# Kernel optimization log

Hardware: AMD Instinct MI355X
Metric: run time of the kernel (lower is better)

Reference implementation:

```python
import jax, jax.numpy as jnp
import numpy as np

D_K = 128  # query/key dim, used for the 1/sqrt(d_k) scale


def setup_inputs() -> dict:
    key = jax.random.key(0)
    k1, k2, k3, k4 = jax.random.split(key, 4)
    B, L, d_model, d_k, d_v = 4, 2048, 1024, 128, 128

    def xavier(k, shape):
        # matches nn.init.xavier_uniform_ for 2D weights
        limit = np.sqrt(6.0 / (shape[0] + shape[1]))
        return jax.random.uniform(k, shape, jnp.float32, -limit, limit)

    return {
        "X": jax.random.normal(k1, (B, L, d_model), jnp.float32),
        "W_Q": xavier(k2, (d_model, d_k)),
        "W_K": xavier(k3, (d_model, d_k)),
        "W_V": xavier(k4, (d_model, d_v)),
    }


def reference(X, W_Q, W_K, W_V):
    # X: (B, L, d_model)
    L = X.shape[1]
    Q = jnp.einsum("bld,dk->blk", X, W_Q)          # (B, L, d_k)
    K = jnp.einsum("bld,dk->blk", X, W_K)          # (B, L, d_k)
    V = jnp.einsum("bld,dv->blv", X, W_V)          # (B, L, d_v)
    scale = D_K ** -0.5
    scores = jnp.einsum("bqk,bpk->bqp", Q, K) * scale  # (B, L, L)
    # causal mask: positions above the diagonal set to -inf
    causal = jnp.tril(jnp.ones((L, L), dtype=bool))
    scores = jnp.where(causal, scores, -jnp.inf)
    A = jax.nn.softmax(scores, axis=-1)            # (B, L, L)
    Z = jnp.einsum("bqp,bpv->bqv", A, V)           # (B, L, d_v)
    return Z
```

## Files before the change

kernel.cpp:

```cpp
#include <hip/hip_runtime.h>
#include <hip/hip_bf16.h>

typedef __bf16 bf16;
typedef __attribute__((ext_vector_type(4))) __bf16 bf16x4;
typedef __attribute__((ext_vector_type(8))) __bf16 bf16x8;
typedef __attribute__((ext_vector_type(4))) float f32x4;

#define D_MODEL 1024
#define DK 128
#define LSEQ 2048
#define NQT 128
#define NB 4
#define SCALE2 (0.08838834764831845f * 1.4426950408889634f)

__global__ __launch_bounds__(256) void wt_kernel(
    const float* __restrict__ Wq, const float* __restrict__ Wk,
    const float* __restrict__ Wv, bf16* __restrict__ Wt)
{
    __shared__ bf16 tile[64][72];
    const float* W = (blockIdx.z == 0) ? Wq : (blockIdx.z == 1) ? Wk : Wv;
    int k0 = blockIdx.x * 64;
    int n0 = blockIdx.y * 64;
    int t  = threadIdx.x;
    #pragma unroll
    for (int i = 0; i < 16; ++i) {
        int idx = t + i * 256;
        int r = idx >> 6, c = idx & 63;
        tile[c][r] = (bf16)W[(size_t)(k0 + r) * DK + n0 + c];
    }
    __syncthreads();
    bf16* out = Wt + (size_t)blockIdx.z * DK * D_MODEL;
    #pragma unroll
    for (int i = 0; i < 16; ++i) {
        int idx = t + i * 256;
        int rr = idx >> 6, cc = idx & 63;
        out[(size_t)(n0 + rr) * D_MODEL + k0 + cc] = tile[rr][cc];
    }
}

__global__ __launch_bounds__(256) void proj_kernel(
    const float* __restrict__ X, const bf16* __restrict__ Wt,
    bf16* __restrict__ Qs, bf16* __restrict__ Kb, bf16* __restrict__ Vt)
{
    __shared__ bf16 Xs[64][72];
    __shared__ bf16 Ws[128][72];
    int mt = blockIdx.x, mat = blockIdx.y;
    const bf16* W = Wt + (size_t)mat * DK * D_MODEL;
    int t = threadIdx.x;
    int wave = t >> 6, lane = t & 63;
    int lq = lane & 15, g = lane >> 4;
    int row0 = mt * 64;

    f32x4 acc[4][2];
    #pragma unroll
    for (int m = 0; m < 4; ++m)
        #pragma unroll
        for (int n = 0; n < 2; ++n) acc[m][n] = f32x4{0.f, 0.f, 0.f, 0.f};

    f32x4  rxf[4];
    bf16x8 rw[4];
    auto LOADR = [&](int k0) {
        #pragma unroll
        for (int i = 0; i < 4; ++i) {
            int u = t + i * 256, r = u >> 4, c4 = u & 15;
            rxf[i] = *reinterpret_cast<const f32x4*>(
                &X[(size_t)(row0 + r) * D_MODEL + k0 + c4 * 4]);
        }
        #pragma unroll
        for (int i = 0; i < 4; ++i) {
            int u = t + i * 256, r = u >> 3, c8 = u & 7;
            rw[i] = *reinterpret_cast<const bf16x8*>(
                &W[(size_t)r * D_MODEL + k0 + c8 * 8]);
        }
    };
    auto STORER = [&]() {
        #pragma unroll
        for (int i = 0; i < 4; ++i) {
            int u = t + i * 256, r = u >> 4, c4 = u & 15;
            bf16x4 h;
            h[0]=(bf16)rxf[i][0]; h[1]=(bf16)rxf[i][1];
            h[2]=(bf16)rxf[i][2]; h[3]=(bf16)rxf[i][3];
            *reinterpret_cast<bf16x4*>(&Xs[r][c4 * 4]) = h;
        }
        #pragma unroll
        for (int i = 0; i < 4; ++i) {
            int u = t + i * 256, r = u >> 3, c8 = u & 7;
            *reinterpret_cast<bf16x8*>(&Ws[r][c8 * 8]) = rw[i];
        }
    };

    LOADR(0);
    for (int ks = 0; ks < 16; ++ks) {
        __syncthreads();
        STORER();
        if (ks + 1 < 16) LOADR((ks + 1) * 64);
        __syncthreads();
        #pragma unroll
        for (int kk = 0; kk < 2; ++kk) {
            bf16x8 a[4];
            #pragma unroll
            for (int mr = 0; mr < 4; ++mr)
                a[mr] = *reinterpret_cast<const bf16x8*>(&Xs[mr * 16 + lq][kk * 32 + g * 8]);
            #pragma unroll
            for (int n = 0; n < 2; ++n) {
                bf16x8 bfr = *reinterpret_cast<const bf16x8*>(
                    &Ws[wave * 32 + n * 16 + lq][kk * 32 + g * 8]);
                #pragma unroll
                for (int mr = 0; mr < 4; ++mr)
                    acc[mr][n] = __builtin_amdgcn_mfma_f32_16x16x32_bf16(a[mr], bfr, acc[mr][n], 0, 0, 0);
            }
        }
    }
    #pragma unroll
    for (int mr = 0; mr < 4; ++mr) {
        int orow = row0 + mr * 16 + g * 4;
        #pragma unroll
        for (int n = 0; n < 2; ++n) {
            int col = wave * 32 + n * 16 + lq;
            if (mat == 0) {
                #pragma unroll
                for (int r = 0; r < 4; ++r)
                    Qs[(size_t)(orow + r) * DK + col] = (bf16)(acc[mr][n][r] * SCALE2);
            } else if (mat == 1) {
                #pragma unroll
                for (int r = 0; r < 4; ++r)
                    Kb[(size_t)(orow + r) * DK + col] = (bf16)acc[mr][n][r];
            } else {
                int bb  = orow >> 11;
                int kv0 = orow & 2047;
                bf16x4 h;
                h[0]=(bf16)acc[mr][n][0]; h[1]=(bf16)acc[mr][n][1];
                h[2]=(bf16)acc[mr][n][2]; h[3]=(bf16)acc[mr][n][3];
                *reinterpret_cast<bf16x4*>(
                    &Vt[((size_t)bb * DK + col) * LSEQ + kv0]) = h;
            }
        }
    }
}

__global__ __launch_bounds__(256, 3) void attn_kernel(
    const bf16* __restrict__ Qs, const bf16* __restrict__ Kb,
    const bf16* __restrict__ Vt, float* __restrict__ Zp,
    float* __restrict__ Mp, float* __restrict__ Lp,
    float* __restrict__ Out, int S, int direct)
{
    __shared__ bf16 Ks[64][136];
    __shared__ bf16 Vs[128][72];
    __shared__ bf16 P[4][16][72];
    int bid = blockIdx.x;
    int b, qblk, s;
    if (S == 4) {
        int xcd = bid & 7, n = bid >> 3;
        b = xcd >> 1;
        int half = n >> 5, qraw = n & 31;
        qblk = half ? (31 - qraw) : qraw;
        s = ((xcd & 1) << 1) | half;
    } else {
        b = bid / (S * 32);
        int rem = bid % (S * 32);
        qblk = rem & 31;
        s = rem >> 5;
    }
    int t = threadIdx.x;
    int wave = t >> 6, lane = t & 63;
    int lq = lane & 15, g = lane >> 4;
    int qw16 = qblk * 4 + wave;
    int qg = qw16 * 16 + lq;

    int nt  = qblk + 1;
    int cpt = (nt + S - 1) / S;
    int t0  = s * cpt;
    int t1  = min(t0 + cpt, nt);

    const bf16* Kbase = Kb + (size_t)b * LSEQ * DK;
    const bf16* Vbase = Vt + (size_t)b * DK * LSEQ;

    const bf16* Qrow = Qs + ((size_t)b * LSEQ + qg) * DK;
    bf16x8 qf[4];
    #pragma unroll
    for (int ks = 0; ks < 4; ++ks)
        qf[ks] = *reinterpret_cast<const bf16x8*>(&Qrow[ks * 32 + g * 8]);

    f32x4 z[8];
    #pragma unroll
    for (int i = 0; i < 8; ++i) z[i] = f32x4{0.f, 0.f, 0.f, 0.f};
    float mrun = -3.0e38f, lrun = 0.f;

    bf16x8 kreg[4], vreg[4];
    auto LOADKV = [&](int kvb) {
        #pragma unroll
        for (int i = 0; i < 4; ++i) {
            int u = t + i * 256, r = u >> 4, c = u & 15;
            kreg[i] = *reinterpret_cast<const bf16x8*>(
                &Kbase[(size_t)(kvb + r) * DK + c * 8]);
        }
        #pragma unroll
        for (int i = 0; i < 4; ++i) {
            int u = t + i * 256, d = u >> 3, c = u & 7;
            vreg[i] = *reinterpret_cast<const bf16x8*>(
                &Vbase[(size_t)d * LSEQ + kvb + c * 8]);
        }
    };
    auto STOREKV = [&]() {
        #pragma unroll
        for (int i = 0; i < 4; ++i) {
            int u = t + i * 256, r = u >> 4, c = u & 15;
            *reinterpret_cast<bf16x8*>(&Ks[r][c * 8]) = kreg[i];
        }
        #pragma unroll
        for (int i = 0; i < 4; ++i) {
            int u = t + i * 256, d = u >> 3, c = u & 7;
            *reinterpret_cast<bf16x8*>(&Vs[d][c * 8]) = vreg[i];
        }
    };

    if (t0 < t1) {
        LOADKV(t0 * 64);
        for (int ti = t0; ti < t1; ++ti) {
            int kvb = ti * 64;
            __syncthreads();
            STOREKV();
            if (ti + 1 < t1) LOADKV((ti + 1) * 64);
            __syncthreads();

            f32x4 sc[4];
            #pragma unroll
            for (int jj = 0; jj < 4; ++jj) sc[jj] = f32x4{0.f, 0.f, 0.f, 0.f};
            __builtin_amdgcn_s_setprio(1);
            #pragma unroll
            for (int jj = 0; jj < 4; ++jj)
                #pragma unroll
                for (int ks = 0; ks < 4; ++ks) {
                    bf16x8 a = *reinterpret_cast<const bf16x8*>(
                        &Ks[jj * 16 + lq][ks * 32 + g * 8]);
                    sc[jj] = __builtin_amdgcn_mfma_f32_16x16x32_bf16(a, qf[ks], sc[jj], 0, 0, 0);
                }
            __builtin_amdgcn_s_setprio(0);

            float sv[16];
            if (ti == nt - 1) {
                #pragma unroll
                for (int jj = 0; jj < 4; ++jj)
                    #pragma unroll
                    for (int r = 0; r < 4; ++r) {
                        int kv0 = kvb + jj * 16 + g * 4 + r;
                        sv[jj * 4 + r] = (kv0 <= qg) ? sc[jj][r] : -3.0e38f;
                    }
            } else {
                #pragma unroll
                for (int jj = 0; jj < 4; ++jj)
                    #pragma unroll
                    for (int r = 0; r < 4; ++r) sv[jj * 4 + r] = sc[jj][r];
            }
            float mt = sv[0];
            #pragma unroll
            for (int i = 1; i < 16; ++i) mt = fmaxf(mt, sv[i]);
            mt = fmaxf(mt, __shfl_xor(mt, 16));
            mt = fmaxf(mt, __shfl_xor(mt, 32));
            if (!__all(mt <= mrun)) {
                float mnew  = fmaxf(mrun, mt);
                float alpha = exp2f(mrun - mnew);
                lrun *= alpha;
                #pragma unroll
                for (int i = 0; i < 8; ++i) {
                    z[i][0] *= alpha; z[i][1] *= alpha; z[i][2] *= alpha; z[i][3] *= alpha;
                }
                mrun = mnew;
            }
            float psum = 0.f;
            #pragma unroll
            for (int jj = 0; jj < 4; ++jj) {
                bf16x4 pb;
                #pragma unroll
                for (int r = 0; r < 4; ++r) {
                    float e = exp2f(sv[jj * 4 + r] - mrun);
                    psum += e;
                    pb[r] = (bf16)e;
                }
                *reinterpret_cast<bf16x4*>(&P[wave][lq][jj * 16 + g * 4]) = pb;
            }
            psum += __shfl_xor(psum, 16);
            psum += __shfl_xor(psum, 32);
            lrun += psum;
            __builtin_amdgcn_s_setprio(1);
            #pragma unroll
            for (int sl = 0; sl < 2; ++sl) {
                bf16x8 pf = *reinterpret_cast<const bf16x8*>(&P[wave][lq][sl * 32 + g * 8]);
                #pragma unroll
                for (int dt = 0; dt < 8; ++dt) {
                    bf16x8 av = *reinterpret_cast<const bf16x8*>(
                        &Vs[dt * 16 + lq][sl * 32 + g * 8]);
                    z[dt] = __builtin_amdgcn_mfma_f32_16x16x32_bf16(av, pf, z[dt], 0, 0, 0);
                }
            }
            __builtin_amdgcn_s_setprio(0);
        }
    }

    if (direct) {
        float inv = 1.f / lrun;
        float* orow = Out + ((size_t)b * LSEQ + qg) * DK;
        #pragma unroll
        for (int dt = 0; dt < 8; ++dt) {
            f32x4 v;
            v[0]=z[dt][0]*inv; v[1]=z[dt][1]*inv; v[2]=z[dt][2]*inv; v[3]=z[dt][3]*inv;
            *reinterpret_cast<f32x4*>(&orow[dt * 16 + g * 4]) = v;
        }
    } else {
        size_t T = ((size_t)(b * NQT + qw16) * S + s);
        float* zp = Zp + T * (16 * 128);
        #pragma unroll
        for (int dt = 0; dt < 8; ++dt)
            *reinterpret_cast<f32x4*>(&zp[lq * 128 + dt * 16 + g * 4]) = z[dt];
        if (g == 0) {
            Mp[T * 16 + lq] = mrun;
            Lp[T * 16 + lq] = lrun;
        }
    }
}

__global__ __launch_bounds__(256) void combine_kernel(
    const float* __restrict__ Zp, const float* __restrict__ Mp,
    const float* __restrict__ Lp, float* __restrict__ Out, int S)
{
    int qt = blockIdx.x, b = blockIdx.y;
    int t  = threadIdx.x;
    int r  = t >> 4;
    int d0 = (t & 15) * 8;
    size_t Tbase = (size_t)(b * NQT + qt) * S;

    float m = -3.0e38f;
    for (int s = 0; s < S; ++s)
        m = fmaxf(m, Mp[(Tbase + s) * 16 + r]);

    float L = 0.f;
    f32x4 a0 = {0.f,0.f,0.f,0.f}, a1 = {0.f,0.f,0.f,0.f};
    for (int s = 0; s < S; ++s) {
        float w = exp2f(Mp[(Tbase + s) * 16 + r] - m);
        L += w * Lp[(Tbase + s) * 16 + r];
        const float* zp = Zp + (Tbase + s) * (16 * 128) + r * 128 + d0;
        f32x4 v0 = *reinterpret_cast<const f32x4*>(&zp[0]);
        f32x4 v1 = *reinterpret_cast<const f32x4*>(&zp[4]);
        a0[0]+=w*v0[0]; a0[1]+=w*v0[1]; a0[2]+=w*v0[2]; a0[3]+=w*v0[3];
        a1[0]+=w*v1[0]; a1[1]+=w*v1[1]; a1[2]+=w*v1[2]; a1[3]+=w*v1[3];
    }
    float inv = 1.f / L;
    float* orow = Out + ((size_t)b * LSEQ + qt * 16 + r) * DK + d0;
    f32x4 o0, o1;
    o0[0]=a0[0]*inv; o0[1]=a0[1]*inv; o0[2]=a0[2]*inv; o0[3]=a0[3]*inv;
    o1[0]=a1[0]*inv; o1[1]=a1[1]*inv; o1[2]=a1[2]*inv; o1[3]=a1[3]*inv;
    *reinterpret_cast<f32x4*>(&orow[0]) = o0;
    *reinterpret_cast<f32x4*>(&orow[4]) = o1;
}

extern "C" void kernel_launch(void* const* d_in, const int* in_sizes, int n_in,
                              void* d_out, int out_size, void* d_ws, size_t ws_size,
                              hipStream_t stream)
{
    const float* X  = (const float*)d_in[0];
    const float* Wq = (const float*)d_in[1];
    const float* Wk = (const float*)d_in[2];
    const float* Wv = (const float*)d_in[3];
    float* Out = (float*)d_out;

    char* ws = (char*)d_ws;
    bf16* Wt = (bf16*)(ws);
    bf16* Qs = (bf16*)(ws + ((size_t)1 << 20));
    bf16* Kb = (bf16*)(ws + ((size_t)3 << 20));
    bf16* Vt = (bf16*)(ws + ((size_t)5 << 20));
    size_t base = (size_t)7 << 20;

    auto need = [](int S) -> size_t {
        return ((size_t)7 << 20) + (size_t)S * ((size_t)NB * NQT * 16 * 128 * 4)
                                 + (size_t)S * 2 * ((size_t)NB * NQT * 16 * 4);
    };
    int S = 1;
    if      (ws_size >= need(4)) S = 4;
    else if (ws_size >= need(2)) S = 2;

    float* Zp = (float*)(ws + base);
    float* Mp = (float*)(ws + base + (size_t)S * NB * NQT * 16 * 128 * 4);
    float* Lp = (float*)(ws + base + (size_t)S * NB * NQT * 16 * 128 * 4
                                   + (size_t)S * NB * NQT * 16 * 4);

    hipLaunchKernelGGL(wt_kernel,   dim3(16, 2, 3), dim3(256), 0, stream, Wq, Wk, Wv, Wt);
    hipLaunchKernelGGL(proj_kernel, dim3(128, 3),   dim3(256), 0, stream, X, Wt, Qs, Kb, Vt);
    hipLaunchKernelGGL(attn_kernel, dim3(S * 32 * NB), dim3(256), 0, stream,
                       Qs, Kb, Vt, Zp, Mp, Lp, Out, S, (S == 1) ? 1 : 0);
    if (S > 1)
        hipLaunchKernelGGL(combine_kernel, dim3(NQT, NB), dim3(256), 0, stream,
                           Zp, Mp, Lp, Out, S);
}
```

Before: 51.77 us.

## Rework attention around 32x32 MFMA with double-buffered async LDS loads and swizzled K/V

The attention kernel now uses 128-thread blocks of two waves, each handling 32 query rows with 32x32x16 bf16 MFMAs in place of 16x16x32. K/V tiles are staged straight into double-buffered LDS with global_load_lds, replacing the register round-trip and removing one barrier per iteration. The projection kernel writes K and V^T with an XOR swizzle so the unpadded LDS tiles read without bank conflicts. The combine kernel and partial-result layout are reshaped for 64-row query tiles. Costs are fewer waves per block, higher register pressure from the larger accumulators, and reliance on the barrier waiting for the async LDS loads to finish.

New measurement: 63.66 us. 1.23x slower.

```diff
diff --git a/kernel.cpp b/kernel.cpp
--- a/kernel.cpp
+++ b/kernel.cpp
@@ -5,13 +5,17 @@
 typedef __attribute__((ext_vector_type(4))) __bf16 bf16x4;
 typedef __attribute__((ext_vector_type(8))) __bf16 bf16x8;
 typedef __attribute__((ext_vector_type(4))) float f32x4;
+typedef __attribute__((ext_vector_type(16))) float f32x16;
 
 #define D_MODEL 1024
 #define DK 128
 #define LSEQ 2048
-#define NQT 128
 #define NB 4
 #define SCALE2 (0.08838834764831845f * 1.4426950408889634f)
+
+#define GLD16(g, l) __builtin_amdgcn_global_load_lds(                       \
+    (const __attribute__((address_space(1))) void*)(g),                     \
+    (__attribute__((address_space(3))) void*)(l), 16, 0, 0)
 
 __global__ __launch_bounds__(256) void wt_kernel(
     const float* __restrict__ Wq, const float* __restrict__ Wk,
@@ -122,31 +126,37 @@
                 for (int r = 0; r < 4; ++r)
                     Qs[(size_t)(orow + r) * DK + col] = (bf16)(acc[mr][n][r] * SCALE2);
             } else if (mat == 1) {
-                #pragma unroll
-                for (int r = 0; r < 4; ++r)
-                    Kb[(size_t)(orow + r) * DK + col] = (bf16)acc[mr][n][r];
+                int colg = col >> 3, cre = col & 7;
+                #pragma unroll
+                for (int r = 0; r < 4; ++r) {
+                    int row = orow + r;
+                    Kb[(size_t)row * DK + ((colg ^ (row & 7)) << 3) + cre]
+                        = (bf16)acc[mr][n][r];
+                }
             } else {
                 int bb  = orow >> 11;
                 int kv0 = orow & 2047;
+                int gv  = ((kv0 & 63) >> 3) ^ (col & 7);
                 bf16x4 h;
                 h[0]=(bf16)acc[mr][n][0]; h[1]=(bf16)acc[mr][n][1];
                 h[2]=(bf16)acc[mr][n][2]; h[3]=(bf16)acc[mr][n][3];
                 *reinterpret_cast<bf16x4*>(
-                    &Vt[((size_t)bb * DK + col) * LSEQ + kv0]) = h;
+                    &Vt[((size_t)bb * DK + col) * LSEQ + (kv0 & ~63) + (gv << 3) + (kv0 & 7)]) = h;
             }
         }
     }
 }
 
-__global__ __launch_bounds__(256, 3) void attn_kernel(
+__global__ __launch_bounds__(128, 2) void attn_kernel(
     const bf16* __restrict__ Qs, const bf16* __restrict__ Kb,
     const bf16* __restrict__ Vt, float* __restrict__ Zp,
     float* __restrict__ Mp, float* __restrict__ Lp,
     float* __restrict__ Out, int S, int direct)
 {
-    __shared__ bf16 Ks[64][136];
-    __shared__ bf16 Vs[128][72];
-    __shared__ bf16 P[4][16][72];
+    __shared__ __align__(16) bf16 Ks[2][64][128];
+    __shared__ __align__(16) bf16 Vs[2][128][64];
+    __shared__ __align__(16) bf16 Pw[2][32][72];
+
     int bid = blockIdx.x;
     int b, qblk, s;
     if (S == 4) {
@@ -163,9 +173,9 @@
     }
     int t = threadIdx.x;
     int wave = t >> 6, lane = t & 63;
-    int lq = lane & 15, g = lane >> 4;
-    int qw16 = qblk * 4 + wave;
-    int qg = qw16 * 16 + lq;
+    int l31 = lane & 31, hi = lane >> 5;
+    int qg  = qblk * 64 + wave * 32 + l31;
+    int swz = l31 & 7;
 
     int nt  = qblk + 1;
     int cpt = (nt + S - 1) / S;
@@ -176,124 +186,122 @@
     const bf16* Vbase = Vt + (size_t)b * DK * LSEQ;
 
     const bf16* Qrow = Qs + ((size_t)b * LSEQ + qg) * DK;
-    bf16x8 qf[4];
-    #pragma unroll
-    for (int ks = 0; ks < 4; ++ks)
-        qf[ks] = *reinterpret_cast<const bf16x8*>(&Qrow[ks * 32 + g * 8]);
-
-    f32x4 z[8];
-    #pragma unroll
-    for (int i = 0; i < 8; ++i) z[i] = f32x4{0.f, 0.f, 0.f, 0.f};
+    bf16x8 qf[8];
+    #pragma unroll
+    for (int ks = 0; ks < 8; ++ks)
+        qf[ks] = *reinterpret_cast<const bf16x8*>(&Qrow[ks * 16 + hi * 8]);
+
+    f32x16 z[4];
+    #pragma unroll
+    for (int db = 0; db < 4; ++db)
+        #pragma unroll
+        for (int r = 0; r < 16; ++r) z[db][r] = 0.f;
     float mrun = -3.0e38f, lrun = 0.f;
 
-    bf16x8 kreg[4], vreg[4];
-    auto LOADKV = [&](int kvb) {
-        #pragma unroll
-        for (int i = 0; i < 4; ++i) {
-            int u = t + i * 256, r = u >> 4, c = u & 15;
-            kreg[i] = *reinterpret_cast<const bf16x8*>(
-                &Kbase[(size_t)(kvb + r) * DK + c * 8]);
-        }
-        #pragma unroll
-        for (int i = 0; i < 4; ++i) {
-            int u = t + i * 256, d = u >> 3, c = u & 7;
-            vreg[i] = *reinterpret_cast<const bf16x8*>(
-                &Vbase[(size_t)d * LSEQ + kvb + c * 8]);
-        }
+    auto STAGE = [&](int buf, int ti) {
+        int kvb = ti * 64;
+        const char* kg = (const char*)(Kbase + (size_t)kvb * DK) + t * 16;
+        char* kl = (char*)(&Ks[buf][0][0]) + t * 16;
+        #pragma unroll
+        for (int i = 0; i < 8; ++i)
+            GLD16(kg + i * 2048, kl + i * 2048);
+        const char* vg = (const char*)Vbase + (size_t)(t >> 3) * (LSEQ * 2)
+                       + (size_t)kvb * 2 + (t & 7) * 16;
+        char* vl = (char*)(&Vs[buf][0][0]) + t * 16;
+        #pragma unroll
+        for (int i = 0; i < 8; ++i)
+            GLD16(vg + (size_t)i * 16 * (LSEQ * 2), vl + i * 2048);
     };
-    auto STOREKV = [&]() {
-        #pragma unroll
-        for (int i = 0; i < 4; ++i) {
-            int u = t + i * 256, r = u >> 4, c = u & 15;
-            *reinterpret_cast<bf16x8*>(&Ks[r][c * 8]) = kreg[i];
-        }
-        #pragma unroll
-        for (int i = 0; i < 4; ++i) {
-            int u = t + i * 256, d = u >> 3, c = u & 7;
-            *reinterpret_cast<bf16x8*>(&Vs[d][c * 8]) = vreg[i];
-        }
-    };
 
     if (t0 < t1) {
-        LOADKV(t0 * 64);
+        STAGE(0, t0);
+        int cur = 0;
         for (int ti = t0; ti < t1; ++ti) {
+            __syncthreads();
+            if (ti + 1 < t1) STAGE(cur ^ 1, ti + 1);
             int kvb = ti * 64;
-            __syncthreads();
-            STOREKV();
-            if (ti + 1 < t1) LOADKV((ti + 1) * 64);
-            __syncthreads();
-
-            f32x4 sc[4];
-            #pragma unroll
-            for (int jj = 0; jj < 4; ++jj) sc[jj] = f32x4{0.f, 0.f, 0.f, 0.f};
+
+            f32x16 sc[2];
+            #pragma unroll
+            for (int jj = 0; jj < 2; ++jj)
+                #pragma unroll
+                for (int r = 0; r < 16; ++r) sc[jj][r] = 0.f;
+
             __builtin_amdgcn_s_setprio(1);
             #pragma unroll
-            for (int jj = 0; jj < 4; ++jj)
-                #pragma unroll
-                for (int ks = 0; ks < 4; ++ks) {
+            for (int jj = 0; jj < 2; ++jj) {
+                const char* kr = (const char*)&Ks[cur][jj * 32 + l31][0];
+                #pragma unroll
+                for (int ks = 0; ks < 8; ++ks) {
                     bf16x8 a = *reinterpret_cast<const bf16x8*>(
-                        &Ks[jj * 16 + lq][ks * 32 + g * 8]);
-                    sc[jj] = __builtin_amdgcn_mfma_f32_16x16x32_bf16(a, qf[ks], sc[jj], 0, 0, 0);
+                        kr + (((2 * ks + hi) ^ swz) << 4));
+                    sc[jj] = __builtin_amdgcn_mfma_f32_32x32x16_bf16(a, qf[ks], sc[jj], 0, 0, 0);
                 }
+            }
             __builtin_amdgcn_s_setprio(0);
 
-            float sv[16];
+            float mt = -3.0e38f;
             if (ti == nt - 1) {
                 #pragma unroll
-                for (int jj = 0; jj < 4; ++jj)
+                for (int jj = 0; jj < 2; ++jj)
                     #pragma unroll
-                    for (int r = 0; r < 4; ++r) {
-                        int kv0 = kvb + jj * 16 + g * 4 + r;
-                        sv[jj * 4 + r] = (kv0 <= qg) ? sc[jj][r] : -3.0e38f;
+                    for (int r = 0; r < 16; ++r) {
+                        int kv0 = kvb + jj * 32 + (r & 3) + 8 * (r >> 2) + 4 * hi;
+                        float v = (kv0 <= qg) ? sc[jj][r] : -3.0e38f;
+                        sc[jj][r] = v;
+                        mt = fmaxf(mt, v);
                     }
             } else {
                 #pragma unroll
-                for (int jj = 0; jj < 4; ++jj)
+                for (int jj = 0; jj < 2; ++jj)
                     #pragma unroll
-                    for (int r = 0; r < 4; ++r) sv[jj * 4 + r] = sc[jj][r];
-            }
-            float mt = sv[0];
-            #pragma unroll
-            for (int i = 1; i < 16; ++i) mt = fmaxf(mt, sv[i]);
-            mt = fmaxf(mt, __shfl_xor(mt, 16));
+                    for (int r = 0; r < 16; ++r) mt = fmaxf(mt, sc[jj][r]);
+            }
             mt = fmaxf(mt, __shfl_xor(mt, 32));
             if (!__all(mt <= mrun)) {
                 float mnew  = fmaxf(mrun, mt);
                 float alpha = exp2f(mrun - mnew);
                 lrun *= alpha;
                 #pragma unroll
-                for (int i = 0; i < 8; ++i) {
-                    z[i][0] *= alpha; z[i][1] *= alpha; z[i][2] *= alpha; z[i][3] *= alpha;
+                for (int db = 0; db < 4; ++db)
+                    #pragma unroll
+                    for (int r = 0; r < 16; ++r) z[db][r] *= alpha;
+                mrun = mnew;
+            }
+            float psum = 0.f;
+            #pragma unroll
+            for (int jj = 0; jj < 2; ++jj) {
+                #pragma unroll
+                for (int rq = 0; rq < 4; ++rq) {
+                    bf16x4 pb;
+                    #pragma unroll
+                    for (int r = 0; r < 4; ++r) {
+                        float e = exp2f(sc[jj][rq * 4 + r] - mrun);
+                        psum += e;
+                        pb[r] = (bf16)e;
+                    }
+                    *reinterpret_cast<bf16x4*>(
+                        &Pw[wave][l31][jj * 32 + rq * 8 + hi * 4]) = pb;
                 }
-                mrun = mnew;
-            }
-            float psum = 0.f;
-            #pragma unroll
-            for (int jj = 0; jj < 4; ++jj) {
-                bf16x4 pb;
-                #pragma unroll
-                for (int r = 0; r < 4; ++r) {
-                    float e = exp2f(sv[jj * 4 + r] - mrun);
-                    psum += e;
-                    pb[r] = (bf16)e;
-                }
-                *reinterpret_cast<bf16x4*>(&P[wave][lq][jj * 16 + g * 4]) = pb;
-            }
-            psum += __shfl_xor(psum, 16);
+            }
             psum += __shfl_xor(psum, 32);
             lrun += psum;
+
             __builtin_amdgcn_s_setprio(1);
             #pragma unroll
-            for (int sl = 0; sl < 2; ++sl) {
-                bf16x8 pf = *reinterpret_cast<const bf16x8*>(&P[wave][lq][sl * 32 + g * 8]);
-                #pragma unroll
-                for (int dt = 0; dt < 8; ++dt) {
-                    bf16x8 av = *reinterpret_cast<const bf16x8*>(
-                        &Vs[dt * 16 + lq][sl * 32 + g * 8]);
-                    z[dt] = __builtin_amdgcn_mfma_f32_16x16x32_bf16(av, pf, z[dt], 0, 0, 0);
+            for (int kc = 0; kc < 4; ++kc) {
+                bf16x8 pb = *reinterpret_cast<const bf16x8*>(
+                    &Pw[wave][l31][kc * 16 + hi * 8]);
+                #pragma unroll
+                for (int db = 0; db < 4; ++db) {
+                    bf16x8 a = *reinterpret_cast<const bf16x8*>(
+                        (const char*)&Vs[cur][db * 32 + l31][0]
+                        + (((2 * kc + hi) ^ swz) << 4));
+                    z[db] = __builtin_amdgcn_mfma_f32_32x32x16_bf16(a, pb, z[db], 0, 0, 0);
                 }
             }
             __builtin_amdgcn_s_setprio(0);
+            cur ^= 1;
         }
     }
 
@@ -301,20 +309,29 @@
         float inv = 1.f / lrun;
         float* orow = Out + ((size_t)b * LSEQ + qg) * DK;
         #pragma unroll
-        for (int dt = 0; dt < 8; ++dt) {
-            f32x4 v;
-            v[0]=z[dt][0]*inv; v[1]=z[dt][1]*inv; v[2]=z[dt][2]*inv; v[3]=z[dt][3]*inv;
-            *reinterpret_cast<f32x4*>(&orow[dt * 16 + g * 4]) = v;
-        }
+        for (int db = 0; db < 4; ++db)
+            #pragma unroll
+            for (int rq = 0; rq < 4; ++rq) {
+                f32x4 v;
+                v[0] = z[db][rq*4+0] * inv; v[1] = z[db][rq*4+1] * inv;
+                v[2] = z[db][rq*4+2] * inv; v[3] = z[db][rq*4+3] * inv;
+                *reinterpret_cast<f32x4*>(&orow[db * 32 + rq * 8 + hi * 4]) = v;
+            }
     } else {
-        size_t T = ((size_t)(b * NQT + qw16) * S + s);
-        float* zp = Zp + T * (16 * 128);
-        #pragma unroll
-        for (int dt = 0; dt < 8; ++dt)
-            *reinterpret_cast<f32x4*>(&zp[lq * 128 + dt * 16 + g * 4]) = z[dt];
-        if (g == 0) {
-            Mp[T * 16 + lq] = mrun;
-            Lp[T * 16 + lq] = lrun;
+        size_t T = (size_t)(b * 32 + qblk) * S + s;
+        float* zp = Zp + T * (64 * 128) + (size_t)(wave * 32 + l31) * 128;
+        #pragma unroll
+        for (int db = 0; db < 4; ++db)
+            #pragma unroll
+            for (int rq = 0; rq < 4; ++rq) {
+                f32x4 v;
+                v[0] = z[db][rq*4+0]; v[1] = z[db][rq*4+1];
+                v[2] = z[db][rq*4+2]; v[3] = z[db][rq*4+3];
+                *reinterpret_cast<f32x4*>(&zp[db * 32 + rq * 8 + hi * 4]) = v;
+            }
+        if (hi == 0) {
+            Mp[T * 64 + wave * 32 + l31] = mrun;
+            Lp[T * 64 + wave * 32 + l31] = lrun;
         }
     }
 }
@@ -325,32 +342,38 @@
 {
     int qt = blockIdx.x, b = blockIdx.y;
     int t  = threadIdx.x;
-    int r  = t >> 4;
-    int d0 = (t & 15) * 8;
-    size_t Tbase = (size_t)(b * NQT + qt) * S;
+    int r  = t & 63;
+    int dc = t >> 6;
+    size_t Tbase = (size_t)(b * 32 + qt) * S;
 
     float m = -3.0e38f;
     for (int s = 0; s < S; ++s)
-        m = fmaxf(m, Mp[(Tbase + s) * 16 + r]);
+        m = fmaxf(m, Mp[(Tbase + s) * 64 + r]);
 
     float L = 0.f;
-    f32x4 a0 = {0.f,0.f,0.f,0.f}, a1 = {0.f,0.f,0.f,0.f};
+    f32x4 a[8];
+    #pragma unroll
+    for (int j = 0; j < 8; ++j) a[j] = f32x4{0.f, 0.f, 0.f, 0.f};
     for (int s = 0; s < S; ++s) {
-        float w = exp2f(Mp[(Tbase + s) * 16 + r] - m);
-        L += w * Lp[(Tbase + s) * 16 + r];
-        const float* zp = Zp + (Tbase + s) * (16 * 128) + r * 128 + d0;
-        f32x4 v0 = *reinterpret_cast<const f32x4*>(&zp[0]);
-        f32x4 v1 = *reinterpret_cast<const f32x4*>(&zp[4]);
-        a0[0]+=w*v0[0]; a0[1]+=w*v0[1]; a0[2]+=w*v0[2]; a0[3]+=w*v0[3];
-        a1[0]+=w*v1[0]; a1[1]+=w*v1[1]; a1[2]+=w*v1[2]; a1[3]+=w*v1[3];
+        float mm = Mp[(Tbase + s) * 64 + r];
+        float w  = exp2f(mm - m);
+        L += w * Lp[(Tbase + s) * 64 + r];
+        const float* zp = Zp + (Tbase + s) * 8192 + (size_t)r * 128 + dc * 32;
+        #pragma unroll
+        for (int j = 0; j < 8; ++j) {
+            f32x4 v = *reinterpret_cast<const f32x4*>(&zp[j * 4]);
+            a[j][0] += w * v[0]; a[j][1] += w * v[1];
+            a[j][2] += w * v[2]; a[j][3] += w * v[3];
+        }
     }
     float inv = 1.f / L;
-    float* orow = Out + ((size_t)b * LSEQ + qt * 16 + r) * DK + d0;
-    f32x4 o0, o1;
-    o0[0]=a0[0]*inv; o0[1]=a0[1]*inv; o0[2]=a0[2]*inv; o0[3]=a0[3]*inv;
-    o1[0]=a1[0]*inv; o1[1]=a1[1]*inv; o1[2]=a1[2]*inv; o1[3]=a1[3]*inv;
-    *reinterpret_cast<f32x4*>(&orow[0]) = o0;
-    *reinterpret_cast<f32x4*>(&orow[4]) = o1;
+    float* orow = Out + ((size_t)b * LSEQ + qt * 64 + r) * DK + dc * 32;
+    #pragma unroll
+    for (int j = 0; j < 8; ++j) {
+        f32x4 o;
+        o[0]=a[j][0]*inv; o[1]=a[j][1]*inv; o[2]=a[j][2]*inv; o[3]=a[j][3]*inv;
+        *reinterpret_cast<f32x4*>(&orow[j * 4]) = o;
+    }
 }
 
 extern "C" void kernel_launch(void* const* d_in, const int* in_sizes, int n_in,
@@ -371,23 +394,24 @@
     size_t base = (size_t)7 << 20;
 
     auto need = [](int S) -> size_t {
-        return ((size_t)7 << 20) + (size_t)S * ((size_t)NB * NQT * 16 * 128 * 4)
-                                 + (size_t)S * 2 * ((size_t)NB * NQT * 16 * 4);
+        return ((size_t)7 << 20)
+             + (size_t)S * ((size_t)NB * 32 * 64 * 128 * 4)
+             + (size_t)S * 2 * ((size_t)NB * 32 * 64 * 4);
     };
     int S = 1;
     if      (ws_size >= need(4)) S = 4;
     else if (ws_size >= need(2)) S = 2;
 
     float* Zp = (float*)(ws + base);
-    float* Mp = (float*)(ws + base + (size_t)S * NB * NQT * 16 * 128 * 4);
-    float* Lp = (float*)(ws + base + (size_t)S * NB * NQT * 16 * 128 * 4
-                                   + (size_t)S * NB * NQT * 16 * 4);
+    float* Mp = (float*)(ws + base + (size_t)S * NB * 32 * 64 * 128 * 4);
+    float* Lp = (float*)(ws + base + (size_t)S * NB * 32 * 64 * 128 * 4
+                                   + (size_t)S * NB * 32 * 64 * 4);
 
     hipLaunchKernelGGL(wt_kernel,   dim3(16, 2, 3), dim3(256), 0, stream, Wq, Wk, Wv, Wt);
     hipLaunchKernelGGL(proj_kernel, dim3(128, 3),   dim3(256), 0, stream, X, Wt, Qs, Kb, Vt);
-    hipLaunchKernelGGL(attn_kernel, dim3(S * 32 * NB), dim3(256), 0, stream,
+    hipLaunchKernelGGL(attn_kernel, dim3(S * 32 * NB), dim3(128), 0, stream,
                        Qs, Kb, Vt, Zp, Mp, Lp, Out, S, (S == 1) ? 1 : 0);
     if (S > 1)
-        hipLaunchKernelGGL(combine_kernel, dim3(NQT, NB), dim3(256), 0, stream,
+        hipLaunchKernelGGL(combine_kernel, dim3(32, NB), dim3(256), 0, stream,
                            Zp, Mp, Lp, Out, S);
 }
```

## Use 128-row query tiles with 8 waves and fixed-size KV chunk splitting

Applied to the files above, without the earlier changes.

The attention kernel moves from 64-row query blocks with 4 waves to 128-row query blocks with 8 waves (512 threads). Each K/V tile loaded into shared memory is now reused by twice as many queries. Work is split into fixed 4-tile KV chunks per block through a triangular index map, which gives 72 blocks per batch with balanced work. The combine kernel is rewritten for the variable number of splits per query block. The trade-offs are fewer, larger blocks, lower occupancy from dropping the 3-blocks-per-CU hint, larger partial buffers, and removal of the XCD-aware block ordering.

Result: slower. 71.34 us (+37.8%).

```diff
diff --git a/kernel.cpp b/kernel.cpp
--- a/kernel.cpp
+++ b/kernel.cpp
@@ -9,7 +9,6 @@
 #define D_MODEL 1024
 #define DK 128
 #define LSEQ 2048
-#define NQT 128
 #define NB 4
 #define SCALE2 (0.08838834764831845f * 1.4426950408889634f)
 
@@ -138,39 +137,38 @@
     }
 }
 
-__global__ __launch_bounds__(256, 3) void attn_kernel(
+__global__ __launch_bounds__(512) void attn_kernel(
     const bf16* __restrict__ Qs, const bf16* __restrict__ Kb,
     const bf16* __restrict__ Vt, float* __restrict__ Zp,
     float* __restrict__ Mp, float* __restrict__ Lp,
-    float* __restrict__ Out, int S, int direct)
+    float* __restrict__ Out, int split)
 {
     __shared__ bf16 Ks[64][136];
     __shared__ bf16 Vs[128][72];
-    __shared__ bf16 P[4][16][72];
+    __shared__ bf16 P[8][16][72];
+
     int bid = blockIdx.x;
-    int b, qblk, s;
-    if (S == 4) {
-        int xcd = bid & 7, n = bid >> 3;
-        b = xcd >> 1;
-        int half = n >> 5, qraw = n & 31;
-        qblk = half ? (31 - qraw) : qraw;
-        s = ((xcd & 1) << 1) | half;
+    int b, qblk, s, t0, t1, nt;
+    if (split) {
+        b = bid / 72;
+        int n = bid % 72;
+        int j = 0;
+        while ((j + 1) * (j + 2) <= n) ++j;
+        int u = n - j * (j + 1);
+        qblk = 2 * j + u / (j + 1);
+        s    = u % (j + 1);
+        nt = 2 * (qblk + 1);
+        t0 = 4 * s;
+        t1 = min(t0 + 4, nt);
     } else {
-        b = bid / (S * 32);
-        int rem = bid % (S * 32);
-        qblk = rem & 31;
-        s = rem >> 5;
-    }
+        b = bid / 16; qblk = bid % 16;
+        s = 0; nt = 2 * (qblk + 1); t0 = 0; t1 = nt;
+    }
+
     int t = threadIdx.x;
     int wave = t >> 6, lane = t & 63;
     int lq = lane & 15, g = lane >> 4;
-    int qw16 = qblk * 4 + wave;
-    int qg = qw16 * 16 + lq;
-
-    int nt  = qblk + 1;
-    int cpt = (nt + S - 1) / S;
-    int t0  = s * cpt;
-    int t1  = min(t0 + cpt, nt);
+    int qg = qblk * 128 + wave * 16 + lq;
 
     const bf16* Kbase = Kb + (size_t)b * LSEQ * DK;
     const bf16* Vbase = Vt + (size_t)b * DK * LSEQ;
@@ -186,118 +184,116 @@
     for (int i = 0; i < 8; ++i) z[i] = f32x4{0.f, 0.f, 0.f, 0.f};
     float mrun = -3.0e38f, lrun = 0.f;
 
-    bf16x8 kreg[4], vreg[4];
+    bf16x8 kreg[2], vreg[2];
     auto LOADKV = [&](int kvb) {
         #pragma unroll
-        for (int i = 0; i < 4; ++i) {
-            int u = t + i * 256, r = u >> 4, c = u & 15;
+        for (int i = 0; i < 2; ++i) {
+            int u = t + i * 512, r = u >> 4, c = u & 15;
             kreg[i] = *reinterpret_cast<const bf16x8*>(
                 &Kbase[(size_t)(kvb + r) * DK + c * 8]);
         }
         #pragma unroll
-        for (int i = 0; i < 4; ++i) {
-            int u = t + i * 256, d = u >> 3, c = u & 7;
+        for (int i = 0; i < 2; ++i) {
+            int u = t + i * 512, d = u >> 3, c = u & 7;
             vreg[i] = *reinterpret_cast<const bf16x8*>(
                 &Vbase[(size_t)d * LSEQ + kvb + c * 8]);
         }
     };
     auto STOREKV = [&]() {
         #pragma unroll
-        for (int i = 0; i < 4; ++i) {
-            int u = t + i * 256, r = u >> 4, c = u & 15;
+        for (int i = 0; i < 2; ++i) {
+            int u = t + i * 512, r = u >> 4, c = u & 15;
             *reinterpret_cast<bf16x8*>(&Ks[r][c * 8]) = kreg[i];
         }
         #pragma unroll
-        for (int i = 0; i < 4; ++i) {
-            int u = t + i * 256, d = u >> 3, c = u & 7;
+        for (int i = 0; i < 2; ++i) {
+            int u = t + i * 512, d = u >> 3, c = u & 7;
             *reinterpret_cast<bf16x8*>(&Vs[d][c * 8]) = vreg[i];
         }
     };
 
-    if (t0 < t1) {
-        LOADKV(t0 * 64);
-        for (int ti = t0; ti < t1; ++ti) {
-            int kvb = ti * 64;
-            __syncthreads();
-            STOREKV();
-            if (ti + 1 < t1) LOADKV((ti + 1) * 64);
-            __syncthreads();
-
-            f32x4 sc[4];
-            #pragma unroll
-            for (int jj = 0; jj < 4; ++jj) sc[jj] = f32x4{0.f, 0.f, 0.f, 0.f};
-            __builtin_amdgcn_s_setprio(1);
+    LOADKV(t0 * 64);
+    for (int ti = t0; ti < t1; ++ti) {
+        int kvb = ti * 64;
+        __syncthreads();
+        STOREKV();
+        if (ti + 1 < t1) LOADKV((ti + 1) * 64);
+        __syncthreads();
+
+        f32x4 sc[4];
+        #pragma unroll
+        for (int jj = 0; jj < 4; ++jj) sc[jj] = f32x4{0.f, 0.f, 0.f, 0.f};
+        __builtin_amdgcn_s_setprio(1);
+        #pragma unroll
+        for (int jj = 0; jj < 4; ++jj)
+            #pragma unroll
+            for (int ks = 0; ks < 4; ++ks) {
+                bf16x8 a = *reinterpret_cast<const bf16x8*>(
+                    &Ks[jj * 16 + lq][ks * 32 + g * 8]);
+                sc[jj] = __builtin_amdgcn_mfma_f32_16x16x32_bf16(a, qf[ks], sc[jj], 0, 0, 0);
+            }
+        __builtin_amdgcn_s_setprio(0);
+
+        float sv[16];
+        if (ti >= nt - 2) {
             #pragma unroll
             for (int jj = 0; jj < 4; ++jj)
                 #pragma unroll
-                for (int ks = 0; ks < 4; ++ks) {
-                    bf16x8 a = *reinterpret_cast<const bf16x8*>(
-                        &Ks[jj * 16 + lq][ks * 32 + g * 8]);
-                    sc[jj] = __builtin_amdgcn_mfma_f32_16x16x32_bf16(a, qf[ks], sc[jj], 0, 0, 0);
+                for (int r = 0; r < 4; ++r) {
+                    int kv0 = kvb + jj * 16 + g * 4 + r;
+                    sv[jj * 4 + r] = (kv0 <= qg) ? sc[jj][r] : -3.0e38f;
                 }
-            __builtin_amdgcn_s_setprio(0);
-
-            float sv[16];
-            if (ti == nt - 1) {
-                #pragma unroll
-                for (int jj = 0; jj < 4; ++jj)
-                    #pragma unroll
-                    for (int r = 0; r < 4; ++r) {
-                        int kv0 = kvb + jj * 16 + g * 4 + r;
-                        sv[jj * 4 + r] = (kv0 <= qg) ? sc[jj][r] : -3.0e38f;
-                    }
-            } else {
-                #pragma unroll
-                for (int jj = 0; jj < 4; ++jj)
-                    #pragma unroll
-                    for (int r = 0; r < 4; ++r) sv[jj * 4 + r] = sc[jj][r];
-            }
-            float mt = sv[0];
-            #pragma unroll
-            for (int i = 1; i < 16; ++i) mt = fmaxf(mt, sv[i]);
-            mt = fmaxf(mt, __shfl_xor(mt, 16));
-            mt = fmaxf(mt, __shfl_xor(mt, 32));
-            if (!__all(mt <= mrun)) {
-                float mnew  = fmaxf(mrun, mt);
-                float alpha = exp2f(mrun - mnew);
-                lrun *= alpha;
-                #pragma unroll
-                for (int i = 0; i < 8; ++i) {
-                    z[i][0] *= alpha; z[i][1] *= alpha; z[i][2] *= alpha; z[i][3] *= alpha;
-                }
-                mrun = mnew;
-            }
-            float psum = 0.f;
-            #pragma unroll
-            for (int jj = 0; jj < 4; ++jj) {
-                bf16x4 pb;
-                #pragma unroll
-                for (int r = 0; r < 4; ++r) {
-                    float e = exp2f(sv[jj * 4 + r] - mrun);
-                    psum += e;
-                    pb[r] = (bf16)e;
-                }
-                *reinterpret_cast<bf16x4*>(&P[wave][lq][jj * 16 + g * 4]) = pb;
-            }
-            psum += __shfl_xor(psum, 16);
-            psum += __shfl_xor(psum, 32);
-            lrun += psum;
-            __builtin_amdgcn_s_setprio(1);
-            #pragma unroll
-            for (int sl = 0; sl < 2; ++sl) {
-                bf16x8 pf = *reinterpret_cast<const bf16x8*>(&P[wave][lq][sl * 32 + g * 8]);
-                #pragma unroll
-                for (int dt = 0; dt < 8; ++dt) {
-                    bf16x8 av = *reinterpret_cast<const bf16x8*>(
-                        &Vs[dt * 16 + lq][sl * 32 + g * 8]);
-                    z[dt] = __builtin_amdgcn_mfma_f32_16x16x32_bf16(av, pf, z[dt], 0, 0, 0);
-                }
-            }
-            __builtin_amdgcn_s_setprio(0);
-        }
-    }
-
-    if (direct) {
+        } else {
+            #pragma unroll
+            for (int jj = 0; jj < 4; ++jj)
+                #pragma unroll
+                for (int r = 0; r < 4; ++r) sv[jj * 4 + r] = sc[jj][r];
+        }
+        float mt = sv[0];
+        #pragma unroll
+        for (int i = 1; i < 16; ++i) mt = fmaxf(mt, sv[i]);
+        mt = fmaxf(mt, __shfl_xor(mt, 16));
+        mt = fmaxf(mt, __shfl_xor(mt, 32));
+        if (!__all(mt <= mrun)) {
+            float mnew  = fmaxf(mrun, mt);
+            float alpha = exp2f(mrun - mnew);
+            lrun *= alpha;
+            #pragma unroll
+            for (int i = 0; i < 8; ++i) {
+                z[i][0] *= alpha; z[i][1] *= alpha; z[i][2] *= alpha; z[i][3] *= alpha;
+            }
+            mrun = mnew;
+        }
+        float psum = 0.f;
+        #pragma unroll
+        for (int jj = 0; jj < 4; ++jj) {
+            bf16x4 pb;
+            #pragma unroll
+            for (int r = 0; r < 4; ++r) {
+                float e = exp2f(sv[jj * 4 + r] - mrun);
+                psum += e;
+                pb[r] = (bf16)e;
+            }
+            *reinterpret_cast<bf16x4*>(&P[wave][lq][jj * 16 + g * 4]) = pb;
+        }
+        psum += __shfl_xor(psum, 16);
+        psum += __shfl_xor(psum, 32);
+        lrun += psum;
+        __builtin_amdgcn_s_setprio(1);
+        #pragma unroll
+        for (int sl = 0; sl < 2; ++sl) {
+            bf16x8 pf = *reinterpret_cast<const bf16x8*>(&P[wave][lq][sl * 32 + g * 8]);
+            #pragma unroll
+            for (int dt = 0; dt < 8; ++dt) {
+                bf16x8 av = *reinterpret_cast<const bf16x8*>(
+                    &Vs[dt * 16 + lq][sl * 32 + g * 8]);
+                z[dt] = __builtin_amdgcn_mfma_f32_16x16x32_bf16(av, pf, z[dt], 0, 0, 0);
+            }
+        }
+        __builtin_amdgcn_s_setprio(0);
+    }
+
+    if (!split) {
         float inv = 1.f / lrun;
         float* orow = Out + ((size_t)b * LSEQ + qg) * DK;
         #pragma unroll
@@ -307,50 +303,57 @@
             *reinterpret_cast<f32x4*>(&orow[dt * 16 + g * 4]) = v;
         }
     } else {
-        size_t T = ((size_t)(b * NQT + qw16) * S + s);
-        float* zp = Zp + T * (16 * 128);
+        size_t T = ((size_t)(b * 16 + qblk) * 8 + s);
+        int rloc = wave * 16 + lq;
+        float* zp = Zp + T * (128 * 128) + (size_t)rloc * 128;
         #pragma unroll
         for (int dt = 0; dt < 8; ++dt)
-            *reinterpret_cast<f32x4*>(&zp[lq * 128 + dt * 16 + g * 4]) = z[dt];
+            *reinterpret_cast<f32x4*>(&zp[dt * 16 + g * 4]) = z[dt];
         if (g == 0) {
-            Mp[T * 16 + lq] = mrun;
-            Lp[T * 16 + lq] = lrun;
-        }
-    }
-}
-
-__global__ __launch_bounds__(256) void combine_kernel(
+            Mp[T * 128 + rloc] = mrun;
+            Lp[T * 128 + rloc] = lrun;
+        }
+    }
+}
+
+__global__ __launch_bounds__(512) void combine_kernel(
     const float* __restrict__ Zp, const float* __restrict__ Mp,
-    const float* __restrict__ Lp, float* __restrict__ Out, int S)
-{
-    int qt = blockIdx.x, b = blockIdx.y;
+    const float* __restrict__ Lp, float* __restrict__ Out)
+{
+    int qblk = blockIdx.x, b = blockIdx.y;
+    int S = (qblk >> 1) + 1;
     int t  = threadIdx.x;
-    int r  = t >> 4;
-    int d0 = (t & 15) * 8;
-    size_t Tbase = (size_t)(b * NQT + qt) * S;
+    int r  = t >> 2;
+    int d0 = (t & 3) * 32;
+    size_t Tbase = (size_t)(b * 16 + qblk) * 8;
 
     float m = -3.0e38f;
     for (int s = 0; s < S; ++s)
-        m = fmaxf(m, Mp[(Tbase + s) * 16 + r]);
+        m = fmaxf(m, Mp[(Tbase + s) * 128 + r]);
 
     float L = 0.f;
-    f32x4 a0 = {0.f,0.f,0.f,0.f}, a1 = {0.f,0.f,0.f,0.f};
+    f32x4 a[8];
+    #pragma unroll
+    for (int j = 0; j < 8; ++j) a[j] = f32x4{0.f, 0.f, 0.f, 0.f};
     for (int s = 0; s < S; ++s) {
-        float w = exp2f(Mp[(Tbase + s) * 16 + r] - m);
-        L += w * Lp[(Tbase + s) * 16 + r];
-        const float* zp = Zp + (Tbase + s) * (16 * 128) + r * 128 + d0;
-        f32x4 v0 = *reinterpret_cast<const f32x4*>(&zp[0]);
-        f32x4 v1 = *reinterpret_cast<const f32x4*>(&zp[4]);
-        a0[0]+=w*v0[0]; a0[1]+=w*v0[1]; a0[2]+=w*v0[2]; a0[3]+=w*v0[3];
-        a1[0]+=w*v1[0]; a1[1]+=w*v1[1]; a1[2]+=w*v1[2]; a1[3]+=w*v1[3];
+        float w = exp2f(Mp[(Tbase + s) * 128 + r] - m);
+        L += w * Lp[(Tbase + s) * 128 + r];
+        const float* zp = Zp + (Tbase + s) * (128 * 128) + (size_t)r * 128 + d0;
+        #pragma unroll
+        for (int j = 0; j < 8; ++j) {
+            f32x4 v = *reinterpret_cast<const f32x4*>(&zp[j * 4]);
+            a[j][0] += w * v[0]; a[j][1] += w * v[1];
+            a[j][2] += w * v[2]; a[j][3] += w * v[3];
+        }
     }
     float inv = 1.f / L;
-    float* orow = Out + ((size_t)b * LSEQ + qt * 16 + r) * DK + d0;
-    f32x4 o0, o1;
-    o0[0]=a0[0]*inv; o0[1]=a0[1]*inv; o0[2]=a0[2]*inv; o0[3]=a0[3]*inv;
-    o1[0]=a1[0]*inv; o1[1]=a1[1]*inv; o1[2]=a1[2]*inv; o1[3]=a1[3]*inv;
-    *reinterpret_cast<f32x4*>(&orow[0]) = o0;
-    *reinterpret_cast<f32x4*>(&orow[4]) = o1;
+    float* orow = Out + ((size_t)b * LSEQ + qblk * 128 + r) * DK + d0;
+    #pragma unroll
+    for (int j = 0; j < 8; ++j) {
+        f32x4 o;
+        o[0]=a[j][0]*inv; o[1]=a[j][1]*inv; o[2]=a[j][2]*inv; o[3]=a[j][3]*inv;
+        *reinterpret_cast<f32x4*>(&orow[j * 4]) = o;
+    }
 }
 
 extern "C" void kernel_launch(void* const* d_in, const int* in_sizes, int n_in,
@@ -368,26 +371,22 @@
     bf16* Qs = (bf16*)(ws + ((size_t)1 << 20));
     bf16* Kb = (bf16*)(ws + ((size_t)3 << 20));
     bf16* Vt = (bf16*)(ws + ((size_t)5 << 20));
+
+    size_t zp_bytes = (size_t)NB * 16 * 8 * 128 * 128 * 4;
+    size_t ml_bytes = (size_t)NB * 16 * 8 * 128 * 4;
     size_t base = (size_t)7 << 20;
-
-    auto need = [](int S) -> size_t {
-        return ((size_t)7 << 20) + (size_t)S * ((size_t)NB * NQT * 16 * 128 * 4)
-                                 + (size_t)S * 2 * ((size_t)NB * NQT * 16 * 4);
-    };
-    int S = 1;
-    if      (ws_size >= need(4)) S = 4;
-    else if (ws_size >= need(2)) S = 2;
+    size_t need = base + zp_bytes + 2 * ml_bytes;
+    int split = (ws_size >= need) ? 1 : 0;
 
     float* Zp = (float*)(ws + base);
-    float* Mp = (float*)(ws + base + (size_t)S * NB * NQT * 16 * 128 * 4);
-    float* Lp = (float*)(ws + base + (size_t)S * NB * NQT * 16 * 128 * 4
-                                   + (size_t)S * NB * NQT * 16 * 4);
+    float* Mp = (float*)(ws + base + zp_bytes);
+    float* Lp = (float*)(ws + base + zp_bytes + ml_bytes);
 
     hipLaunchKernelGGL(wt_kernel,   dim3(16, 2, 3), dim3(256), 0, stream, Wq, Wk, Wv, Wt);
     hipLaunchKernelGGL(proj_kernel, dim3(128, 3),   dim3(256), 0, stream, X, Wt, Qs, Kb, Vt);
-    hipLaunchKernelGGL(attn_kernel, dim3(S * 32 * NB), dim3(256), 0, stream,
-                       Qs, Kb, Vt, Zp, Mp, Lp, Out, S, (S == 1) ? 1 : 0);
-    if (S > 1)
-        hipLaunchKernelGGL(combine_kernel, dim3(NQT, NB), dim3(256), 0, stream,
-                           Zp, Mp, Lp, Out, S);
-}
+    hipLaunchKernelGGL(attn_kernel, dim3(split ? NB * 72 : NB * 16), dim3(512), 0, stream,
+                       Qs, Kb, Vt, Zp, Mp, Lp, Out, split);
+    if (split)
+        hipLaunchKernelGGL(combine_kernel, dim3(16, NB), dim3(512), 0, stream,
+                           Zp, Mp, Lp, Out);
+}
```

## Split causal attention into fixed four-tile KV chunks with variable splits per query block

Applied to the files above, without the earlier changes.

The attention grid no longer gives every query block four splits of uneven size. Each work item now covers at most four 64-key tiles, so a query block gets qblk/4+1 splits and the grid has 576 blocks. Blocks are mapped to batch and XCD with a small linear search, and the combine kernel derives the split count from the query tile. The goal is a shorter critical path per block and a more even load across CUs. In exchange it needs a workspace sized for eight partials per tile, adds partial-result traffic, and falls back to the unsplit path if the workspace is too small.

After: 51.88 us. About the same (+0.2%).

```diff
diff --git a/kernel.cpp b/kernel.cpp
--- a/kernel.cpp
+++ b/kernel.cpp
@@ -142,24 +142,25 @@
     const bf16* __restrict__ Qs, const bf16* __restrict__ Kb,
     const bf16* __restrict__ Vt, float* __restrict__ Zp,
     float* __restrict__ Mp, float* __restrict__ Lp,
-    float* __restrict__ Out, int S, int direct)
+    float* __restrict__ Out, int split)
 {
     __shared__ bf16 Ks[64][136];
     __shared__ bf16 Vs[128][72];
     __shared__ bf16 P[4][16][72];
     int bid = blockIdx.x;
     int b, qblk, s;
-    if (S == 4) {
-        int xcd = bid & 7, n = bid >> 3;
+    if (split) {
+        int xcd = bid & 7, u = bid >> 3;
         b = xcd >> 1;
-        int half = n >> 5, qraw = n & 31;
-        qblk = half ? (31 - qraw) : qraw;
-        s = ((xcd & 1) << 1) | half;
+        int n2 = (u << 1) | (xcd & 1);
+        int q = 0, off = 0;
+        while (off + ((q >> 2) + 1) <= n2) { off += (q >> 2) + 1; ++q; }
+        qblk = q;
+        s = n2 - off;
     } else {
-        b = bid / (S * 32);
-        int rem = bid % (S * 32);
-        qblk = rem & 31;
-        s = rem >> 5;
+        b = bid >> 5;
+        qblk = bid & 31;
+        s = 0;
     }
     int t = threadIdx.x;
     int wave = t >> 6, lane = t & 63;
@@ -167,10 +168,9 @@
     int qw16 = qblk * 4 + wave;
     int qg = qw16 * 16 + lq;
 
-    int nt  = qblk + 1;
-    int cpt = (nt + S - 1) / S;
-    int t0  = s * cpt;
-    int t1  = min(t0 + cpt, nt);
+    int nt = qblk + 1;
+    int t0 = split ? 4 * s : 0;
+    int t1 = split ? min(4 * s + 4, nt) : nt;
 
     const bf16* Kbase = Kb + (size_t)b * LSEQ * DK;
     const bf16* Vbase = Vt + (size_t)b * DK * LSEQ;
@@ -214,90 +214,88 @@
         }
     };
 
-    if (t0 < t1) {
-        LOADKV(t0 * 64);
-        for (int ti = t0; ti < t1; ++ti) {
-            int kvb = ti * 64;
-            __syncthreads();
-            STOREKV();
-            if (ti + 1 < t1) LOADKV((ti + 1) * 64);
-            __syncthreads();
-
-            f32x4 sc[4];
-            #pragma unroll
-            for (int jj = 0; jj < 4; ++jj) sc[jj] = f32x4{0.f, 0.f, 0.f, 0.f};
-            __builtin_amdgcn_s_setprio(1);
+    LOADKV(t0 * 64);
+    for (int ti = t0; ti < t1; ++ti) {
+        int kvb = ti * 64;
+        __syncthreads();
+        STOREKV();
+        if (ti + 1 < t1) LOADKV((ti + 1) * 64);
+        __syncthreads();
+
+        f32x4 sc[4];
+        #pragma unroll
+        for (int jj = 0; jj < 4; ++jj) sc[jj] = f32x4{0.f, 0.f, 0.f, 0.f};
+        __builtin_amdgcn_s_setprio(1);
+        #pragma unroll
+        for (int jj = 0; jj < 4; ++jj)
+            #pragma unroll
+            for (int ks = 0; ks < 4; ++ks) {
+                bf16x8 a = *reinterpret_cast<const bf16x8*>(
+                    &Ks[jj * 16 + lq][ks * 32 + g * 8]);
+                sc[jj] = __builtin_amdgcn_mfma_f32_16x16x32_bf16(a, qf[ks], sc[jj], 0, 0, 0);
+            }
+        __builtin_amdgcn_s_setprio(0);
+
+        float sv[16];
+        if (ti == nt - 1) {
             #pragma unroll
             for (int jj = 0; jj < 4; ++jj)
                 #pragma unroll
-                for (int ks = 0; ks < 4; ++ks) {
-                    bf16x8 a = *reinterpret_cast<const bf16x8*>(
-                        &Ks[jj * 16 + lq][ks * 32 + g * 8]);
-                    sc[jj] = __builtin_amdgcn_mfma_f32_16x16x32_bf16(a, qf[ks], sc[jj], 0, 0, 0);
+                for (int r = 0; r < 4; ++r) {
+                    int kv0 = kvb + jj * 16 + g * 4 + r;
+                    sv[jj * 4 + r] = (kv0 <= qg) ? sc[jj][r] : -3.0e38f;
                 }
-            __builtin_amdgcn_s_setprio(0);
-
-            float sv[16];
-            if (ti == nt - 1) {
-                #pragma unroll
-                for (int jj = 0; jj < 4; ++jj)
-                    #pragma unroll
-                    for (int r = 0; r < 4; ++r) {
-                        int kv0 = kvb + jj * 16 + g * 4 + r;
-                        sv[jj * 4 + r] = (kv0 <= qg) ? sc[jj][r] : -3.0e38f;
-                    }
-            } else {
-                #pragma unroll
-                for (int jj = 0; jj < 4; ++jj)
-                    #pragma unroll
-                    for (int r = 0; r < 4; ++r) sv[jj * 4 + r] = sc[jj][r];
-            }
-            float mt = sv[0];
-            #pragma unroll
-            for (int i = 1; i < 16; ++i) mt = fmaxf(mt, sv[i]);
-            mt = fmaxf(mt, __shfl_xor(mt, 16));
-            mt = fmaxf(mt, __shfl_xor(mt, 32));
-            if (!__all(mt <= mrun)) {
-                float mnew  = fmaxf(mrun, mt);
-                float alpha = exp2f(mrun - mnew);
-                lrun *= alpha;
-                #pragma unroll
-                for (int i = 0; i < 8; ++i) {
-                    z[i][0] *= alpha; z[i][1] *= alpha; z[i][2] *= alpha; z[i][3] *= alpha;
-                }
-                mrun = mnew;
-            }
-            float psum = 0.f;
-            #pragma unroll
-            for (int jj = 0; jj < 4; ++jj) {
-                bf16x4 pb;
-                #pragma unroll
-                for (int r = 0; r < 4; ++r) {
-                    float e = exp2f(sv[jj * 4 + r] - mrun);
-                    psum += e;
-                    pb[r] = (bf16)e;
-                }
-                *reinterpret_cast<bf16x4*>(&P[wave][lq][jj * 16 + g * 4]) = pb;
-            }
-            psum += __shfl_xor(psum, 16);
-            psum += __shfl_xor(psum, 32);
-            lrun += psum;
-            __builtin_amdgcn_s_setprio(1);
-            #pragma unroll
-            for (int sl = 0; sl < 2; ++sl) {
-                bf16x8 pf = *reinterpret_cast<const bf16x8*>(&P[wave][lq][sl * 32 + g * 8]);
-                #pragma unroll
-                for (int dt = 0; dt < 8; ++dt) {
-                    bf16x8 av = *reinterpret_cast<const bf16x8*>(
-                        &Vs[dt * 16 + lq][sl * 32 + g * 8]);
-                    z[dt] = __builtin_amdgcn_mfma_f32_16x16x32_bf16(av, pf, z[dt], 0, 0, 0);
-                }
-            }
-            __builtin_amdgcn_s_setprio(0);
-        }
-    }
-
-    if (direct) {
+        } else {
+            #pragma unroll
+            for (int jj = 0; jj < 4; ++jj)
+                #pragma unroll
+                for (int r = 0; r < 4; ++r) sv[jj * 4 + r] = sc[jj][r];
+        }
+        float mt = sv[0];
+        #pragma unroll
+        for (int i = 1; i < 16; ++i) mt = fmaxf(mt, sv[i]);
+        mt = fmaxf(mt, __shfl_xor(mt, 16));
+        mt = fmaxf(mt, __shfl_xor(mt, 32));
+        if (!__all(mt <= mrun)) {
+            float mnew  = fmaxf(mrun, mt);
+            float alpha = exp2f(mrun - mnew);
+            lrun *= alpha;
+            #pragma unroll
+            for (int i = 0; i < 8; ++i) {
+                z[i][0] *= alpha; z[i][1] *= alpha; z[i][2] *= alpha; z[i][3] *= alpha;
+            }
+            mrun = mnew;
+        }
+        float psum = 0.f;
+        #pragma unroll
+        for (int jj = 0; jj < 4; ++jj) {
+            bf16x4 pb;
+            #pragma unroll
+            for (int r = 0; r < 4; ++r) {
+                float e = exp2f(sv[jj * 4 + r] - mrun);
+                psum += e;
+                pb[r] = (bf16)e;
+            }
+            *reinterpret_cast<bf16x4*>(&P[wave][lq][jj * 16 + g * 4]) = pb;
+        }
+        psum += __shfl_xor(psum, 16);
+        psum += __shfl_xor(psum, 32);
+        lrun += psum;
+        __builtin_amdgcn_s_setprio(1);
+        #pragma unroll
+        for (int sl = 0; sl < 2; ++sl) {
+            bf16x8 pf = *reinterpret_cast<const bf16x8*>(&P[wave][lq][sl * 32 + g * 8]);
+            #pragma unroll
+            for (int dt = 0; dt < 8; ++dt) {
+                bf16x8 av = *reinterpret_cast<const bf16x8*>(
+                    &Vs[dt * 16 + lq][sl * 32 + g * 8]);
+                z[dt] = __builtin_amdgcn_mfma_f32_16x16x32_bf16(av, pf, z[dt], 0, 0, 0);
+            }
+        }
+        __builtin_amdgcn_s_setprio(0);
+    }
+
+    if (!split) {
         float inv = 1.f / lrun;
         float* orow = Out + ((size_t)b * LSEQ + qg) * DK;
         #pragma unroll
@@ -307,7 +305,7 @@
             *reinterpret_cast<f32x4*>(&orow[dt * 16 + g * 4]) = v;
         }
     } else {
-        size_t T = ((size_t)(b * NQT + qw16) * S + s);
+        size_t T = ((size_t)(b * NQT + qw16) * 8 + s);
         float* zp = Zp + T * (16 * 128);
         #pragma unroll
         for (int dt = 0; dt < 8; ++dt)
@@ -321,13 +319,14 @@
 
 __global__ __launch_bounds__(256) void combine_kernel(
     const float* __restrict__ Zp, const float* __restrict__ Mp,
-    const float* __restrict__ Lp, float* __restrict__ Out, int S)
+    const float* __restrict__ Lp, float* __restrict__ Out)
 {
     int qt = blockIdx.x, b = blockIdx.y;
+    int S  = (qt >> 4) + 1;
     int t  = threadIdx.x;
     int r  = t >> 4;
     int d0 = (t & 15) * 8;
-    size_t Tbase = (size_t)(b * NQT + qt) * S;
+    size_t Tbase = (size_t)(b * NQT + qt) * 8;
 
     float m = -3.0e38f;
     for (int s = 0; s < S; ++s)
@@ -370,24 +369,19 @@
     bf16* Vt = (bf16*)(ws + ((size_t)5 << 20));
     size_t base = (size_t)7 << 20;
 
-    auto need = [](int S) -> size_t {
-        return ((size_t)7 << 20) + (size_t)S * ((size_t)NB * NQT * 16 * 128 * 4)
-                                 + (size_t)S * 2 * ((size_t)NB * NQT * 16 * 4);
-    };
-    int S = 1;
-    if      (ws_size >= need(4)) S = 4;
-    else if (ws_size >= need(2)) S = 2;
+    size_t zp_bytes = (size_t)NB * NQT * 8 * 16 * 128 * 4;
+    size_t ml_bytes = (size_t)NB * NQT * 8 * 16 * 4;
+    int split = (ws_size >= base + zp_bytes + 2 * ml_bytes) ? 1 : 0;
 
     float* Zp = (float*)(ws + base);
-    float* Mp = (float*)(ws + base + (size_t)S * NB * NQT * 16 * 128 * 4);
-    float* Lp = (float*)(ws + base + (size_t)S * NB * NQT * 16 * 128 * 4
-                                   + (size_t)S * NB * NQT * 16 * 4);
+    float* Mp = (float*)(ws + base + zp_bytes);
+    float* Lp = (float*)(ws + base + zp_bytes + ml_bytes);
 
     hipLaunchKernelGGL(wt_kernel,   dim3(16, 2, 3), dim3(256), 0, stream, Wq, Wk, Wv, Wt);
     hipLaunchKernelGGL(proj_kernel, dim3(128, 3),   dim3(256), 0, stream, X, Wt, Qs, Kb, Vt);
-    hipLaunchKernelGGL(attn_kernel, dim3(S * 32 * NB), dim3(256), 0, stream,
-                       Qs, Kb, Vt, Zp, Mp, Lp, Out, S, (S == 1) ? 1 : 0);
-    if (S > 1)
+    hipLaunchKernelGGL(attn_kernel, dim3(split ? 576 : NB * 32), dim3(256), 0, stream,
+                       Qs, Kb, Vt, Zp, Mp, Lp, Out, split);
+    if (split)
         hipLaunchKernelGGL(combine_kernel, dim3(NQT, NB), dim3(256), 0, stream,
-                           Zp, Mp, Lp, Out, S);
-}
+                           Zp, Mp, Lp, Out);
+}
```
